# Kernel tuning notes

Hardware: AMD Instinct MI355X
Metric: run time of the kernel (lower is better)

Reference implementation:

```python
import jax, jax.numpy as jnp
import numpy as np

NX, NQ, NU, NY = 256, 256, 64, 64
EPS, ALPHA = 1e-3, 0.0
B = 32768


def setup_inputs() -> dict:
    key = jax.random.key(0)
    ks = jax.random.split(key, 8)
    std = np.float32(0.1 / np.sqrt(NX))
    return {
        "t": 0,
        "xi": jax.random.normal(ks[0], (B, NX), jnp.float32),
        "u": jax.random.normal(ks[1], (B, NU), jnp.float32),
        "Pstar": jax.random.normal(ks[2], (NX, NX), jnp.float32) * std,
        "Chi": jax.random.normal(ks[3], (NX, NQ), jnp.float32) * std,
        "Y1": jax.random.normal(ks[4], (NX, NX), jnp.float32) * std,
        "B2": jax.random.normal(ks[5], (NX, NU), jnp.float32) * std,
        "D12": jax.random.normal(ks[6], (NQ, NU), jnp.float32) * std,
        "X": jax.random.normal(ks[7], (NX + NQ, NX + NQ), jnp.float32) * std,
        "bx": jnp.zeros((NX,), jnp.float32),
        "bv": jnp.zeros((NQ,), jnp.float32),
    }


def _constrained_matrices(Pstar, Chi, Y1, X):
    # P = 0.5 Pstar Pstar^T + eps I ; H = X X^T + eps I
    P = 0.5 * (Pstar @ Pstar.T) + EPS * jnp.eye(NX, dtype=Pstar.dtype)
    H = X @ X.T + EPS * jnp.eye(NX + NQ, dtype=X.dtype)
    H1 = H[:NX, :NX]          # [nx,nx]
    H2 = H[:NX, NX:]          # [nx,nq]
    H4 = H[NX:, NX:]          # [nq,nq]
    Y = -0.5 * (H1 + ALPHA * P + Y1 - Y1.T)
    lam_inv = 1.0 / (0.5 * jnp.diagonal(H4))     # inverse of diagonal Lambda
    P_inv = jnp.linalg.inv(P)
    A = P_inv @ Y                                 # F.linear(P_inv, Y.T)
    D11 = -(lam_inv[:, None] * jnp.tril(H4, -1))  # strictly lower triangular [nq,nq]
    C1 = lam_inv[:, None] * Chi.T                 # [nq,nx]
    Z = -H2 - Chi
    B1 = P_inv @ Z                                # [nx,nq]
    return A, B1, C1, D11


def _compute_w(xi, u, C1, D11, D12, bv):
    # v_base[:, i] = xi @ C1[i] + u @ D12[i] + bv[i]  (all steps at once)
    v_base = xi @ C1.T + u @ D12.T + bv           # [B,nq]
    w0 = jnp.zeros_like(v_base)

    def step(w, i):
        # D11 row i is zero for j >= i, and w[:, j>=i] is still zero, so a full
        # matvec exactly reproduces the triangular forward substitution.
        v = v_base[:, i] + w @ D11[i]
        return w.at[:, i].set(jnp.tanh(v)), None

    w, _ = jax.lax.scan(step, w0, jnp.arange(NQ))
    return w


def reference(t, xi, u, Pstar, Chi, Y1, B2, D12, X, bx, bv):
    A, B1, C1, D11 = _constrained_matrices(Pstar, Chi, Y1, X)
    w = _compute_w(xi, u, C1, D11, D12, bv)       # [B,nq]
    xi_dot = xi @ A.T + w @ B1.T + u @ B2.T + bx  # [B,nx]
    return xi_dot
```

## Files before the change

### kernel.cpp

```cpp
#include <hip/hip_runtime.h>
#include <math.h>

#define NXC 256
#define NQC 256
#define NUC 64
#define NHC 512
#define BR  32768
#define EPSC 1e-3f
#define NAUG 768

typedef _Float16 h2_t __attribute__((ext_vector_type(2)));
typedef _Float16 f16x8 __attribute__((ext_vector_type(8)));
typedef float f32x4 __attribute__((ext_vector_type(4)));
union h2u { h2_t h; unsigned int u; };

__device__ __forceinline__ h2_t pk_f16(float a, float b) {
#if __has_builtin(__builtin_amdgcn_cvt_pkrtz)
  return __builtin_bit_cast(h2_t, __builtin_amdgcn_cvt_pkrtz(a, b));
#else
  h2_t r; r.x = (_Float16)a; r.y = (_Float16)b; return r;
#endif
}
__device__ __forceinline__ unsigned int pk_bits(float a, float b) { h2u x; x.h = pk_f16(a, b); return x.u; }
__device__ __forceinline__ h2_t b2h(unsigned int u) { h2u x; x.u = u; return x.h; }
__device__ __forceinline__ unsigned int h2b(h2_t v) { h2u x; x.h = v; return x.u; }

__device__ __forceinline__ float fdot2f(h2_t a, h2_t b, float c) {
#if __has_builtin(__builtin_amdgcn_fdot2)
  return __builtin_amdgcn_fdot2(a, b, c, false);
#else
  return c + (float)a.x * (float)b.x + (float)a.y * (float)b.y;
#endif
}

__device__ __forceinline__ float fast_tanh(float x) {
  float ax = fabsf(x);
  float e  = __expf(-2.0f * ax);
  float r  = __fdividef(1.0f - e, 1.0f + e);
  return copysignf(r, x);
}

__device__ __forceinline__ float fast_rcp(float x) {
#if __has_builtin(__builtin_amdgcn_rcpf)
  return __builtin_amdgcn_rcpf(x);
#else
  return 1.0f / x;
#endif
}

__device__ __forceinline__ void inv32_wave(float r[32], int ii) {
#pragma unroll
  for (int k = 0; k < 32; ++k) {
    float rk[32];
#pragma unroll
    for (int j = 0; j < 32; ++j) rk[j] = __shfl(r[j], k);
    float d = fast_rcp(rk[k]);
    float fik = r[k];
    if (ii == k) {
#pragma unroll
      for (int j = 0; j < 32; ++j) r[j] = (j == k) ? d : rk[j] * d;
    } else {
#pragma unroll
      for (int j = 0; j < 32; ++j) r[j] = (j == k) ? (-fik * d) : (r[j] - fik * (d * rk[j]));
    }
  }
}

__global__ __launch_bounds__(256) void cvt2_kernel(const float* __restrict__ xi,
                                                   const float* __restrict__ u,
                                                   _Float16* __restrict__ xi16,
                                                   _Float16* __restrict__ u16) {
  const int nxi = BR * NXC / 8, ntot = nxi + BR * NUC / 8;
  int idx = blockIdx.x * 256 + threadIdx.x;
  int stride = gridDim.x * 256;
  for (int i = idx; i < ntot; i += stride) {
    const float* s; _Float16* d; int j;
    if (i < nxi) { s = xi; d = xi16; j = i; } else { s = u; d = u16; j = i - nxi; }
    float4 a = ((const float4*)s)[(size_t)j * 2];
    float4 b = ((const float4*)s)[(size_t)j * 2 + 1];
    uint4 o;
    o.x = pk_bits(a.x, a.y); o.y = pk_bits(a.z, a.w);
    o.z = pk_bits(b.x, b.y); o.w = pk_bits(b.z, b.w);
    ((uint4*)d)[j] = o;
  }
}

__global__ __launch_bounds__(256) void syrk_mfma_kernel(const float* __restrict__ Xin,
                                                        const float* __restrict__ Pstar,
                                                        float* __restrict__ Hm,
                                                        float* __restrict__ Naug) {
  __shared__ _Float16 Alds[128][72];
  __shared__ _Float16 Blds[64][72];
  const int b = blockIdx.x, t = threadIdx.x;
  const float* src; float* dst; int n, K; float scale; int rowbase, colbase;
  if (b < 32) { src = Xin;   dst = Hm;   n = NHC;  K = NHC; scale = 1.0f; rowbase = (b >> 3) * 128; colbase = (b & 7) * 64; }
  else { int b2 = b - 32; src = Pstar; dst = Naug; n = NAUG; K = NXC; scale = 0.5f; rowbase = (b2 >> 2) * 128; colbase = (b2 & 3) * 64; }
  const int r_a = t >> 1, h_a = t & 1;
  const int r_b = t >> 2, q_b = t & 3;
  const int lane = t & 63, wv = t >> 6;
  const int wm = wv >> 1, wn = wv & 1;
  const int l15 = lane & 15, l4 = lane >> 4;
  f32x4 acc[4][2] = {};
  for (int k0 = 0; k0 < K; k0 += 64) {
    uint4 av[4], bvv[2];
    {
      const float* p = src + (size_t)(rowbase + r_a) * K + k0 + h_a * 32;
#pragma unroll
      for (int m = 0; m < 4; m++) {
        float4 x0 = *(const float4*)(p + m * 8);
        float4 x1 = *(const float4*)(p + m * 8 + 4);
        uint4 pk;
        pk.x = pk_bits(x0.x, x0.y); pk.y = pk_bits(x0.z, x0.w);
        pk.z = pk_bits(x1.x, x1.y); pk.w = pk_bits(x1.z, x1.w);
        av[m] = pk;
      }
    }
    {
      const float* p = src + (size_t)(colbase + r_b) * K + k0 + q_b * 16;
      float4 x0 = *(const float4*)p,       x1 = *(const float4*)(p + 4);
      float4 x2 = *(const float4*)(p + 8), x3 = *(const float4*)(p + 12);
      bvv[0].x = pk_bits(x0.x, x0.y); bvv[0].y = pk_bits(x0.z, x0.w);
      bvv[0].z = pk_bits(x1.x, x1.y); bvv[0].w = pk_bits(x1.z, x1.w);
      bvv[1].x = pk_bits(x2.x, x2.y); bvv[1].y = pk_bits(x2.z, x2.w);
      bvv[1].z = pk_bits(x3.x, x3.y); bvv[1].w = pk_bits(x3.z, x3.w);
    }
    __syncthreads();
#pragma unroll
    for (int m = 0; m < 4; m++) *(uint4*)&Alds[r_a][h_a * 32 + m * 8] = av[m];
    *(uint4*)&Blds[r_b][q_b * 16]     = bvv[0];
    *(uint4*)&Blds[r_b][q_b * 16 + 8] = bvv[1];
    __syncthreads();
#pragma unroll
    for (int ks = 0; ks < 2; ks++) {
      f16x8 af[4], bf[2];
#pragma unroll
      for (int fm = 0; fm < 4; fm++)
        af[fm] = *(const f16x8*)&Alds[wm * 64 + fm * 16 + l15][ks * 32 + l4 * 8];
#pragma unroll
      for (int fn = 0; fn < 2; fn++)
        bf[fn] = *(const f16x8*)&Blds[wn * 32 + fn * 16 + l15][ks * 32 + l4 * 8];
#pragma unroll
      for (int fm = 0; fm < 4; fm++)
#pragma unroll
        for (int fn = 0; fn < 2; fn++)
          acc[fm][fn] = __builtin_amdgcn_mfma_f32_16x16x32_f16(af[fm], bf[fn], acc[fm][fn], 0, 0, 0);
    }
  }
#pragma unroll
  for (int fm = 0; fm < 4; fm++)
#pragma unroll
    for (int fn = 0; fn < 2; fn++) {
      int col = colbase + wn * 32 + fn * 16 + l15;
      f32x4 a = acc[fm][fn];
#pragma unroll
      for (int reg = 0; reg < 4; reg++) {
        int row = rowbase + wm * 64 + fm * 16 + l4 * 4 + reg;
        float val = scale * a[reg] + ((row == col) ? EPSC : 0.f);
        dst[(size_t)row * n + col] = val;
      }
    }
}

__global__ __launch_bounds__(256) void derive_kernel(const float* __restrict__ H,
                                                     const float* __restrict__ Y1,
                                                     const float* __restrict__ Chi,
                                                     const float* __restrict__ D12,
                                                     const float* __restrict__ B2,
                                                     float* __restrict__ Naug,
                                                     unsigned int* __restrict__ dpk_g,
                                                     _Float16* __restrict__ C1h,
                                                     _Float16* __restrict__ D12h,
                                                     _Float16* __restrict__ B2h) {
  int i = blockIdx.x, j = threadIdx.x;
  float li = 2.0f / H[(size_t)(NXC + i) * NHC + NXC + i];
  Naug[(size_t)i * NAUG + NXC + j]     = -0.5f * (H[(size_t)i * NHC + j] + Y1[i * NXC + j] - Y1[j * NXC + i]);
  C1h[i * NXC + j] = (_Float16)(li * Chi[j * NQC + i]);
  Naug[(size_t)i * NAUG + 2 * NXC + j] = -H[(size_t)i * NHC + NXC + j] - Chi[i * NQC + j];
  float dv = (j < i) ? (-li * H[(size_t)(NXC + i) * NHC + NXC + j]) : 0.f;
  float dhi = __shfl_xor(dv, 1);
  if ((j & 1) == 0) dpk_g[(size_t)(j >> 1) * NXC + i] = pk_bits(dv, dhi);
  if (j < NUC) {
    D12h[i * NUC + j] = (_Float16)D12[i * NUC + j];
    B2h[i * NUC + j]  = (_Float16)B2[i * NUC + j];
  }
}

__global__ __launch_bounds__(256) void gjstep_kernel(const float* __restrict__ Nin,
                                                     float* __restrict__ Nout,
                                                     _Float16* __restrict__ Ah,
                                                     _Float16* __restrict__ B1h,
                                                     int k0) {
  __shared__ float Dl[32][33];
  __shared__ float cfl[8][33];
  const int t = threadIdx.x;
  const int row0 = blockIdx.x * 8;
  const bool last = (k0 + 32 == NXC);
  if (t < 64) {
    const int ii = t & 31;
    float r[32];
#pragma unroll
    for (int j = 0; j < 32; ++j) r[j] = Nin[(size_t)(k0 + ii) * NAUG + k0 + j];
    inv32_wave(r, ii);
    if (t < 32) {
#pragma unroll
      for (int j = 0; j < 32; ++j) Dl[ii][j] = r[j];
    }
  }
  __syncthreads();
  {
    const int rr = t >> 5, s = t & 31;
    const int i = row0 + rr;
    float c;
    if (i >= k0 && i < k0 + 32) {
      c = Dl[i - k0][s];
    } else {
      float g = 0.f;
#pragma unroll
      for (int q = 0; q < 32; ++q) g = fmaf(Nin[(size_t)i * NAUG + k0 + q], Dl[q][s], g);
      c = -g;
    }
    cfl[rr][s] = c;
  }
  __syncthreads();
  const int rr = t >> 5;
  const int i = row0 + rr;
  const bool piv = (i >= k0 && i < k0 + 32);
  float cf[32];
#pragma unroll
  for (int s = 0; s < 32; ++s) cf[s] = cfl[rr][s];
  const int c40 = (k0 + 32) >> 2;
  for (int c4 = c40 + (t & 31); c4 < (NAUG >> 2); c4 += 32) {
    float4 acc;
    if (piv) { acc.x = 0.f; acc.y = 0.f; acc.z = 0.f; acc.w = 0.f; }
    else     { acc = *(const float4*)&Nin[(size_t)i * NAUG + c4 * 4]; }
#pragma unroll
    for (int s = 0; s < 32; ++s) {
      float4 pv = *(const float4*)&Nin[(size_t)(k0 + s) * NAUG + c4 * 4];
      acc.x = fmaf(cf[s], pv.x, acc.x);
      acc.y = fmaf(cf[s], pv.y, acc.y);
      acc.z = fmaf(cf[s], pv.z, acc.z);
      acc.w = fmaf(cf[s], pv.w, acc.w);
    }
    if (!last) {
      *(float4*)&Nout[(size_t)i * NAUG + c4 * 4] = acc;
    } else {
      int cc = c4 * 4 - NXC;
      h2_t h0, h1;
      h0.x = (_Float16)acc.x; h0.y = (_Float16)acc.y;
      h1.x = (_Float16)acc.z; h1.y = (_Float16)acc.w;
      uint2 o; o.x = h2b(h0); o.y = h2b(h1);
      if (cc < NXC) *(uint2*)&Ah[(size_t)i * NXC + cc]          = o;
      else          *(uint2*)&B1h[(size_t)i * NXC + (cc - NXC)] = o;
    }
  }
}

__global__ __launch_bounds__(256, 2) void wrec_fused_kernel(
    const _Float16* __restrict__ xi16, const _Float16* __restrict__ u16,
    const _Float16* __restrict__ C1h, const _Float16* __restrict__ D12h,
    const float* __restrict__ bv, const unsigned int* __restrict__ dpk_g,
    const _Float16* __restrict__ Ah, const _Float16* __restrict__ B1h,
    const _Float16* __restrict__ B2h, const float* __restrict__ bx,
    float* __restrict__ out) {
  __shared__ unsigned int pool[14976];
  unsigned int* wlds  = pool;
  unsigned int* dpkT  = pool + 8448;
  unsigned int* tript = pool + 12160;
  float*        vbuf  = (float*)(pool + 12672);

  const int t = threadIdx.x;
  const int r = t >> 2, s = t & 3;
  const int lane = t & 63, w = t >> 6;
  const int l15 = lane & 15, l4 = lane >> 4;
  const size_t rowbase = (size_t)blockIdx.x * 64;
  const _Float16* wl16 = (const _Float16*)wlds;

  f16x8 xi_frag[8], u_frag[2];
  {
    const _Float16* px = xi16 + (rowbase + w * 16 + l15) * NXC + l4 * 8;
#pragma unroll
    for (int kc = 0; kc < 8; ++kc) xi_frag[kc] = *(const f16x8*)(px + kc * 32);
    const _Float16* pu = u16 + (rowbase + w * 16 + l15) * NUC + l4 * 8;
#pragma unroll
    for (int kc = 0; kc < 2; ++kc) u_frag[kc] = *(const f16x8*)(pu + kc * 32);
  }

  h2_t wpk[16];
#pragma unroll
  for (int p = 0; p < 16; ++p) wpk[p] = pk_f16(0.f, 0.f);

  for (int kb = 0; kb < 8; ++kb) {
    const int i0 = kb * 32;
    for (int idx = t; idx < (i0 >> 1) * 32; idx += 256) {
      int cc = idx & 31, jp = idx >> 5;
      dpkT[cc * 116 + jp] = dpk_g[(size_t)jp * NXC + i0 + cc];
    }
    if (t < 128) {
      int jp = t >> 3, iq = t & 7;
      uint4 d4 = *(const uint4*)&dpk_g[(size_t)(i0 / 2 + jp) * NXC + i0 + iq * 4];
      tript[(iq * 4 + 0) * 16 + jp] = d4.x;
      tript[(iq * 4 + 1) * 16 + jp] = d4.y;
      tript[(iq * 4 + 2) * 16 + jp] = d4.z;
      tript[(iq * 4 + 3) * 16 + jp] = d4.w;
    }
    f32x4 acc0, acc1;
    {
      float b0 = bv[i0 + l15], b1 = bv[i0 + 16 + l15];
      acc0[0] = b0; acc0[1] = b0; acc0[2] = b0; acc0[3] = b0;
      acc1[0] = b1; acc1[1] = b1; acc1[2] = b1; acc1[3] = b1;
#pragma unroll
      for (int kc = 0; kc < 8; ++kc) {
        f16x8 bf0 = *(const f16x8*)&C1h[(size_t)(i0 + l15) * NXC + kc * 32 + l4 * 8];
        f16x8 bf1 = *(const f16x8*)&C1h[(size_t)(i0 + 16 + l15) * NXC + kc * 32 + l4 * 8];
        acc0 = __builtin_amdgcn_mfma_f32_16x16x32_f16(xi_frag[kc], bf0, acc0, 0, 0, 0);
        acc1 = __builtin_amdgcn_mfma_f32_16x16x32_f16(xi_frag[kc], bf1, acc1, 0, 0, 0);
      }
#pragma unroll
      for (int kc = 0; kc < 2; ++kc) {
        f16x8 bf0 = *(const f16x8*)&D12h[(size_t)(i0 + l15) * NUC + kc * 32 + l4 * 8];
        f16x8 bf1 = *(const f16x8*)&D12h[(size_t)(i0 + 16 + l15) * NUC + kc * 32 + l4 * 8];
        acc0 = __builtin_amdgcn_mfma_f32_16x16x32_f16(u_frag[kc], bf0, acc0, 0, 0, 0);
        acc1 = __builtin_amdgcn_mfma_f32_16x16x32_f16(u_frag[kc], bf1, acc1, 0, 0, 0);
      }
    }
    __syncthreads();

    for (int ks = 0; ks < kb; ++ks) {
      f16x8 af = *(const f16x8*)&wl16[(size_t)(w * 16 + l15) * 264 + ks * 32 + l4 * 8];
      uint4 b0 = *(const uint4*)&dpkT[(l15) * 116 + ks * 16 + l4 * 4];
      uint4 b1 = *(const uint4*)&dpkT[(16 + l15) * 116 + ks * 16 + l4 * 4];
      acc0 = __builtin_amdgcn_mfma_f32_16x16x32_f16(af, __builtin_bit_cast(f16x8, b0), acc0, 0, 0, 0);
      acc1 = __builtin_amdgcn_mfma_f32_16x16x32_f16(af, __builtin_bit_cast(f16x8, b1), acc1, 0, 0, 0);
    }

#pragma unroll
    for (int reg = 0; reg < 4; ++reg) {
      int rowm = w * 16 + l4 * 4 + reg;
      vbuf[rowm * 36 + l15]      = acc0[reg];
      vbuf[rowm * 36 + 16 + l15] = acc1[reg];
    }

    float wprev = 0.f;
#pragma unroll
    for (int i = 0; i < 32; ++i) {
      const int npairs = (i + 1) >> 1;
      const int nq = (npairs + 3) >> 2;
      float td0 = 0.f, td1 = 0.f;
#pragma unroll
      for (int q = 0; q < nq; ++q) {
        uint4 tq = *(const uint4*)&tript[i * 16 + q * 4];
        td0 = fdot2f(wpk[q * 4 + 0], b2h(tq.x), td0);
        td1 = fdot2f(wpk[q * 4 + 1], b2h(tq.y), td1);
        td0 = fdot2f(wpk[q * 4 + 2], b2h(tq.z), td0);
        td1 = fdot2f(wpk[q * 4 + 3], b2h(tq.w), td1);
      }
      float vi = vbuf[r * 36 + i];
      float wi = fast_tanh(vi + td0 + td1);
      if ((i & 1) == 0) { wprev = wi; wpk[i >> 1] = pk_f16(wi, 0.f); }
      else              { wpk[i >> 1] = pk_f16(wprev, wi); }
    }

    {
      uint4 o;
      o.x = h2b(wpk[s * 4 + 0]); o.y = h2b(wpk[s * 4 + 1]);
      o.z = h2b(wpk[s * 4 + 2]); o.w = h2b(wpk[s * 4 + 3]);
      *(uint4*)&wlds[r * 132 + kb * 16 + s * 4] = o;
    }
    __syncthreads();
  }

  _Float16* Ws = (_Float16*)dpkT;
  f32x4 oacc[16];
#pragma unroll
  for (int ct = 0; ct < 16; ++ct) {
    float bb = bx[ct * 16 + l15];
    oacc[ct][0] = bb; oacc[ct][1] = bb; oacc[ct][2] = bb; oacc[ct][3] = bb;
  }
  uint4 pa, pb, pc, pd;
  {
    const _Float16* p = Ah + (size_t)t * NXC;
    pa = *(const uint4*)p;        pb = *(const uint4*)(p + 8);
    pc = *(const uint4*)(p + 16); pd = *(const uint4*)(p + 24);
  }
#pragma unroll
  for (int rr = 0; rr < 18; ++rr) {
    const int sel = rr < 8 ? 0 : (rr < 16 ? 1 : 2);
    const int kc  = sel == 0 ? rr : (sel == 1 ? rr - 8 : rr - 16);
    __syncthreads();
    *(uint4*)&Ws[t * 40]      = pa;
    *(uint4*)&Ws[t * 40 + 8]  = pb;
    *(uint4*)&Ws[t * 40 + 16] = pc;
    *(uint4*)&Ws[t * 40 + 24] = pd;
    __syncthreads();
    if (rr < 17) {
      const int rs = rr + 1;
      const int s2 = rs < 8 ? 0 : (rs < 16 ? 1 : 2);
      const int k2 = s2 == 0 ? rs : (s2 == 1 ? rs - 8 : rs - 16);
      const _Float16* Wp = s2 == 0 ? Ah : (s2 == 1 ? B1h : B2h);
      const int KK = (s2 == 2) ? NUC : NXC;
      const _Float16* p = Wp + (size_t)t * KK + k2 * 32;
      pa = *(const uint4*)p;        pb = *(const uint4*)(p + 8);
      pc = *(const uint4*)(p + 16); pd = *(const uint4*)(p + 24);
    }
    f16x8 af;
    if (sel == 0)      af = xi_frag[kc];
    else if (sel == 1) af = *(const f16x8*)&wl16[(size_t)(w * 16 + l15) * 264 + kc * 32 + l4 * 8];
    else               af = u_frag[kc];
#pragma unroll
    for (int ct = 0; ct < 16; ++ct) {
      f16x8 bf = *(const f16x8*)&Ws[(ct * 16 + l15) * 40 + l4 * 8];
      oacc[ct] = __builtin_amdgcn_mfma_f32_16x16x32_f16(af, bf, oacc[ct], 0, 0, 0);
    }
  }
#pragma unroll
  for (int ct = 0; ct < 16; ++ct) {
#pragma unroll
    for (int reg = 0; reg < 4; ++reg) {
      int row = (int)rowbase + w * 16 + l4 * 4 + reg;
      out[(size_t)row * NXC + ct * 16 + l15] = oacc[ct][reg];
    }
  }
}

extern "C" void kernel_launch(void* const* d_in, const int* in_sizes, int n_in,
                              void* d_out, int out_size, void* d_ws, size_t ws_size,
                              hipStream_t stream) {
  (void)in_sizes; (void)n_in; (void)out_size; (void)ws_size;
  const float* xi    = (const float*)d_in[1];
  const float* u     = (const float*)d_in[2];
  const float* Pstar = (const float*)d_in[3];
  const float* Chi   = (const float*)d_in[4];
  const float* Y1    = (const float*)d_in[5];
  const float* B2    = (const float*)d_in[6];
  const float* D12   = (const float*)d_in[7];
  const float* Xin   = (const float*)d_in[8];
  const float* bx    = (const float*)d_in[9];
  const float* bv    = (const float*)d_in[10];
  float* out = (float*)d_out;

  float* ws = (float*)d_ws;
  _Float16* xi16 = (_Float16*)ws;
  _Float16* u16  = xi16 + (size_t)BR * NXC;
  float* Hm = (float*)(u16 + (size_t)BR * NUC);
  float* NA = Hm + (size_t)NHC * NHC;
  float* NB = NA + (size_t)NXC * NAUG;
  unsigned int* dpkg = (unsigned int*)(NB + (size_t)NXC * NAUG);
  _Float16* C1h  = (_Float16*)(dpkg + 128 * 256);
  _Float16* D12h = C1h + (size_t)NQC * NXC;
  _Float16* Ah   = D12h + (size_t)NQC * NUC;
  _Float16* B1h  = Ah + (size_t)NXC * NXC;
  _Float16* B2h  = B1h + (size_t)NXC * NQC;

  cvt2_kernel<<<2048, 256, 0, stream>>>(xi, u, xi16, u16);

  syrk_mfma_kernel<<<40, 256, 0, stream>>>(Xin, Pstar, Hm, NA);
  derive_kernel<<<NXC, NXC, 0, stream>>>(Hm, Y1, Chi, D12, B2, NA, dpkg, C1h, D12h, B2h);

  for (int kb = 0; kb < 8; ++kb) {
    const float* Nin = (kb & 1) ? NB : NA;
    float*      Nout = (kb & 1) ? NA : NB;
    gjstep_kernel<<<32, 256, 0, stream>>>(Nin, Nout, Ah, B1h, kb * 32);
  }

  wrec_fused_kernel<<<BR / 64, 256, 0, stream>>>(
      xi16, u16, C1h, D12h, bv, dpkg, Ah, B1h, B2h, bx, out);
}
```

Baseline: 311.2 us.

## Fuse fp16 input conversion into recurrence kernel and double Gauss-Jordan block width

The separate xi/u fp32-to-fp16 conversion kernel is removed. The recurrence kernel now loads fp32 rows and packs them to fp16 fragments in registers, which avoids writing and re-reading a half-precision copy of the inputs. The Gauss-Jordan inversion now eliminates 64 pivots per launch instead of 32, using a 2x2 block Schur-complement formulation. This halves the number of serialized launches, at the cost of more per-block small matrix work and more shared memory.

```diff
diff --git a/kernel.cpp b/kernel.cpp
--- a/kernel.cpp
+++ b/kernel.cpp
@@ -63,25 +63,6 @@
 #pragma unroll
       for (int j = 0; j < 32; ++j) r[j] = (j == k) ? (-fik * d) : (r[j] - fik * (d * rk[j]));
     }
-  }
-}
-
-__global__ __launch_bounds__(256) void cvt2_kernel(const float* __restrict__ xi,
-                                                   const float* __restrict__ u,
-                                                   _Float16* __restrict__ xi16,
-                                                   _Float16* __restrict__ u16) {
-  const int nxi = BR * NXC / 8, ntot = nxi + BR * NUC / 8;
-  int idx = blockIdx.x * 256 + threadIdx.x;
-  int stride = gridDim.x * 256;
-  for (int i = idx; i < ntot; i += stride) {
-    const float* s; _Float16* d; int j;
-    if (i < nxi) { s = xi; d = xi16; j = i; } else { s = u; d = u16; j = i - nxi; }
-    float4 a = ((const float4*)s)[(size_t)j * 2];
-    float4 b = ((const float4*)s)[(size_t)j * 2 + 1];
-    uint4 o;
-    o.x = pk_bits(a.x, a.y); o.y = pk_bits(a.z, a.w);
-    o.z = pk_bits(b.x, b.y); o.w = pk_bits(b.z, b.w);
-    ((uint4*)d)[j] = o;
   }
 }
 
@@ -185,16 +166,16 @@
   }
 }
 
-__global__ __launch_bounds__(256) void gjstep_kernel(const float* __restrict__ Nin,
-                                                     float* __restrict__ Nout,
-                                                     _Float16* __restrict__ Ah,
-                                                     _Float16* __restrict__ B1h,
-                                                     int k0) {
-  __shared__ float Dl[32][33];
-  __shared__ float cfl[8][33];
+__global__ __launch_bounds__(256) void gjstep2_kernel(const float* __restrict__ Nin,
+                                                      float* __restrict__ Nout,
+                                                      _Float16* __restrict__ Ah,
+                                                      _Float16* __restrict__ B1h,
+                                                      int k0) {
+  __shared__ float D0i[32][33], D1i[32][33], Gm[32][33], W0[32][33], Um[32][33], Vm[32][33];
+  __shared__ float cfa[8][33], cfb[8][33], cfc[8][33];
   const int t = threadIdx.x;
   const int row0 = blockIdx.x * 8;
-  const bool last = (k0 + 32 == NXC);
+  const bool last = (k0 + 64 == NXC);
   if (t < 64) {
     const int ii = t & 31;
     float r[32];
@@ -203,43 +184,124 @@
     inv32_wave(r, ii);
     if (t < 32) {
 #pragma unroll
-      for (int j = 0; j < 32; ++j) Dl[ii][j] = r[j];
-    }
-  }
-  __syncthreads();
+      for (int j = 0; j < 32; ++j) D0i[ii][j] = r[j];
+    }
+  } else {
+    int t2 = t - 64;
+    for (int e = t2; e < 256; e += 192) {
+      int q = e >> 3, s0 = (e & 7) * 4;
+      *(float4*)&Um[q][s0] = *(const float4*)&Nin[(size_t)(k0 + q) * NAUG + k0 + 32 + s0];
+      *(float4*)&Vm[q][s0] = *(const float4*)&Nin[(size_t)(k0 + 32 + q) * NAUG + k0 + s0];
+    }
+  }
+  __syncthreads();
+#pragma unroll
+  for (int e = t; e < 1024; e += 256) {
+    int rw = e >> 5, cw = e & 31;
+    float s1 = 0.f, s2 = 0.f;
+#pragma unroll
+    for (int q = 0; q < 32; ++q) {
+      s1 = fmaf(D0i[rw][q], Um[q][cw], s1);
+      s2 = fmaf(Vm[rw][q], D0i[q][cw], s2);
+    }
+    W0[rw][cw] = s1;
+    Gm[rw][cw] = -s2;
+  }
+  __syncthreads();
+#pragma unroll
+  for (int e = t; e < 1024; e += 256) {
+    int rw = e >> 5, cw = e & 31;
+    float s1 = Nin[(size_t)(k0 + 32 + rw) * NAUG + k0 + 32 + cw];
+#pragma unroll
+    for (int q = 0; q < 32; ++q) s1 = fmaf(-Vm[rw][q], W0[q][cw], s1);
+    D1i[rw][cw] = s1;
+  }
+  __syncthreads();
+  if (t < 64) {
+    const int ii = t & 31;
+    float r[32];
+#pragma unroll
+    for (int j = 0; j < 32; ++j) r[j] = D1i[ii][j];
+    inv32_wave(r, ii);
+    if (t < 32) {
+#pragma unroll
+      for (int j = 0; j < 32; ++j) D1i[ii][j] = r[j];
+    }
+  }
+  __syncthreads();
+  const int rr = t >> 5, s = t & 31;
+  const int i = row0 + rr;
+  const int inP0 = (i >= k0 && i < k0 + 32);
+  const int inP1 = (i >= k0 + 32 && i < k0 + 64);
   {
-    const int rr = t >> 5, s = t & 31;
-    const int i = row0 + rr;
     float c;
-    if (i >= k0 && i < k0 + 32) {
-      c = Dl[i - k0][s];
-    } else {
+    if (inP0) c = D0i[i - k0][s];
+    else if (inP1) c = 0.f;
+    else {
       float g = 0.f;
 #pragma unroll
-      for (int q = 0; q < 32; ++q) g = fmaf(Nin[(size_t)i * NAUG + k0 + q], Dl[q][s], g);
+      for (int q = 0; q < 32; ++q) g = fmaf(Nin[(size_t)i * NAUG + k0 + q], D0i[q][s], g);
       c = -g;
     }
-    cfl[rr][s] = c;
-  }
-  __syncthreads();
-  const int rr = t >> 5;
-  const int i = row0 + rr;
-  const bool piv = (i >= k0 && i < k0 + 32);
-  float cf[32];
-#pragma unroll
-  for (int s = 0; s < 32; ++s) cf[s] = cfl[rr][s];
-  const int c40 = (k0 + 32) >> 2;
+    cfa[rr][s] = c;
+  }
+  __syncthreads();
+  {
+    float c;
+    if (inP0) c = W0[i - k0][s];
+    else if (inP1) c = 0.f;
+    else {
+      float g = Nin[(size_t)i * NAUG + k0 + 32 + s];
+#pragma unroll
+      for (int q = 0; q < 32; ++q) g = fmaf(cfa[rr][q], Um[q][s], g);
+      c = g;
+    }
+    cfc[rr][s] = c;
+  }
+  __syncthreads();
+  {
+    float c;
+    if (inP1) c = D1i[i - k0 - 32][s];
+    else {
+      float g = 0.f;
+#pragma unroll
+      for (int q = 0; q < 32; ++q) g = fmaf(cfc[rr][q], D1i[q][s], g);
+      c = -g;
+    }
+    cfb[rr][s] = c;
+  }
+  __syncthreads();
+  {
+    float g = cfa[rr][s];
+#pragma unroll
+    for (int q = 0; q < 32; ++q) g = fmaf(cfb[rr][q], Gm[q][s], g);
+    cfa[rr][s] = g;
+  }
+  __syncthreads();
+  const bool piv = inP0 || inP1;
+  float ca[32], cb[32];
+#pragma unroll
+  for (int q = 0; q < 32; ++q) { ca[q] = cfa[rr][q]; cb[q] = cfb[rr][q]; }
+  const int c40 = (k0 + 64) >> 2;
   for (int c4 = c40 + (t & 31); c4 < (NAUG >> 2); c4 += 32) {
     float4 acc;
     if (piv) { acc.x = 0.f; acc.y = 0.f; acc.z = 0.f; acc.w = 0.f; }
     else     { acc = *(const float4*)&Nin[(size_t)i * NAUG + c4 * 4]; }
 #pragma unroll
-    for (int s = 0; s < 32; ++s) {
-      float4 pv = *(const float4*)&Nin[(size_t)(k0 + s) * NAUG + c4 * 4];
-      acc.x = fmaf(cf[s], pv.x, acc.x);
-      acc.y = fmaf(cf[s], pv.y, acc.y);
-      acc.z = fmaf(cf[s], pv.z, acc.z);
-      acc.w = fmaf(cf[s], pv.w, acc.w);
+    for (int q = 0; q < 32; ++q) {
+      float4 pv = *(const float4*)&Nin[(size_t)(k0 + q) * NAUG + c4 * 4];
+      acc.x = fmaf(ca[q], pv.x, acc.x);
+      acc.y = fmaf(ca[q], pv.y, acc.y);
+      acc.z = fmaf(ca[q], pv.z, acc.z);
+      acc.w = fmaf(ca[q], pv.w, acc.w);
+    }
+#pragma unroll
+    for (int q = 0; q < 32; ++q) {
+      float4 pv = *(const float4*)&Nin[(size_t)(k0 + 32 + q) * NAUG + c4 * 4];
+      acc.x = fmaf(cb[q], pv.x, acc.x);
+      acc.y = fmaf(cb[q], pv.y, acc.y);
+      acc.z = fmaf(cb[q], pv.z, acc.z);
+      acc.w = fmaf(cb[q], pv.w, acc.w);
     }
     if (!last) {
       *(float4*)&Nout[(size_t)i * NAUG + c4 * 4] = acc;
@@ -256,7 +318,7 @@
 }
 
 __global__ __launch_bounds__(256, 2) void wrec_fused_kernel(
-    const _Float16* __restrict__ xi16, const _Float16* __restrict__ u16,
+    const float* __restrict__ xi, const float* __restrict__ u,
     const _Float16* __restrict__ C1h, const _Float16* __restrict__ D12h,
     const float* __restrict__ bv, const unsigned int* __restrict__ dpk_g,
     const _Float16* __restrict__ Ah, const _Float16* __restrict__ B1h,
@@ -277,12 +339,26 @@
 
   f16x8 xi_frag[8], u_frag[2];
   {
-    const _Float16* px = xi16 + (rowbase + w * 16 + l15) * NXC + l4 * 8;
-#pragma unroll
-    for (int kc = 0; kc < 8; ++kc) xi_frag[kc] = *(const f16x8*)(px + kc * 32);
-    const _Float16* pu = u16 + (rowbase + w * 16 + l15) * NUC + l4 * 8;
-#pragma unroll
-    for (int kc = 0; kc < 2; ++kc) u_frag[kc] = *(const f16x8*)(pu + kc * 32);
+    const float* px = xi + (size_t)(rowbase + w * 16 + l15) * NXC + l4 * 8;
+#pragma unroll
+    for (int kc = 0; kc < 8; ++kc) {
+      float4 a = *(const float4*)(px + kc * 32);
+      float4 b = *(const float4*)(px + kc * 32 + 4);
+      uint4 pk;
+      pk.x = pk_bits(a.x, a.y); pk.y = pk_bits(a.z, a.w);
+      pk.z = pk_bits(b.x, b.y); pk.w = pk_bits(b.z, b.w);
+      xi_frag[kc] = __builtin_bit_cast(f16x8, pk);
+    }
+    const float* pu = u + (size_t)(rowbase + w * 16 + l15) * NUC + l4 * 8;
+#pragma unroll
+    for (int kc = 0; kc < 2; ++kc) {
+      float4 a = *(const float4*)(pu + kc * 32);
+      float4 b = *(const float4*)(pu + kc * 32 + 4);
+      uint4 pk;
+      pk.x = pk_bits(a.x, a.y); pk.y = pk_bits(a.z, a.w);
+      pk.z = pk_bits(b.x, b.y); pk.w = pk_bits(b.z, b.w);
+      u_frag[kc] = __builtin_bit_cast(f16x8, pk);
+    }
   }
 
   h2_t wpk[16];
@@ -439,9 +515,7 @@
   float* out = (float*)d_out;
 
   float* ws = (float*)d_ws;
-  _Float16* xi16 = (_Float16*)ws;
-  _Float16* u16  = xi16 + (size_t)BR * NXC;
-  float* Hm = (float*)(u16 + (size_t)BR * NUC);
+  float* Hm = ws;
   float* NA = Hm + (size_t)NHC * NHC;
   float* NB = NA + (size_t)NXC * NAUG;
   unsigned int* dpkg = (unsigned int*)(NB + (size_t)NXC * NAUG);
@@ -451,17 +525,15 @@
   _Float16* B1h  = Ah + (size_t)NXC * NXC;
   _Float16* B2h  = B1h + (size_t)NXC * NQC;
 
-  cvt2_kernel<<<2048, 256, 0, stream>>>(xi, u, xi16, u16);
-
   syrk_mfma_kernel<<<40, 256, 0, stream>>>(Xin, Pstar, Hm, NA);
   derive_kernel<<<NXC, NXC, 0, stream>>>(Hm, Y1, Chi, D12, B2, NA, dpkg, C1h, D12h, B2h);
 
-  for (int kb = 0; kb < 8; ++kb) {
-    const float* Nin = (kb & 1) ? NB : NA;
-    float*      Nout = (kb & 1) ? NA : NB;
-    gjstep_kernel<<<32, 256, 0, stream>>>(Nin, Nout, Ah, B1h, kb * 32);
+  for (int j = 0; j < 4; ++j) {
+    const float* Nin = (j & 1) ? NB : NA;
+    float*      Nout = (j & 1) ? NA : NB;
+    gjstep2_kernel<<<32, 256, 0, stream>>>(Nin, Nout, Ah, B1h, j * 64);
   }
 
   wrec_fused_kernel<<<BR / 64, 256, 0, stream>>>(
-      xi16, u16, C1h, D12h, bv, dpkg, Ah, B1h, B2h, bx, out);
-}
+      xi, u, C1h, D12h, bv, dpkg, Ah, B1h, B2h, bx, out);
+}
```

Result: slower. 395.2 us (+27.0%).
